# Optimization experiments

Measured on AMD Instinct MI355X. Metric: run time of the kernel, lower is better.

The kernel has to match this reference:

```python
import jax, jax.numpy as jnp
import numpy as np

B = 262144      # Monte Carlo samples (batch)
DH = 128        # d_hidden
DM = 4          # concatenated input feature dim (two one-hot spins)


def _glorot(key, shape):
    fan_in, fan_out = shape[0], shape[1]
    lim = jnp.sqrt(6.0 / (fan_in + fan_out)).astype(jnp.float32)
    return jax.random.uniform(key, shape, jnp.float32, -lim, lim)


def setup_inputs() -> dict:
    key = jax.random.key(0)
    ks = jax.random.split(key, 10)
    inputs = jax.random.normal(ks[0], (B, DM), jnp.float32)
    h1 = jax.random.normal(ks[1], (B, DH), jnp.float32)
    h2 = jax.random.normal(ks[2], (B, DH), jnp.float32)
    U1 = _glorot(ks[3], (DH, DH))
    U2 = _glorot(ks[4], (DH, DH))
    # flax GRUCell params: input kernels (with bias), hidden kernels
    # (r,z: no bias; n: bias). Packed as [ir|iz|in] and [hr|hz].
    Wi = _glorot(ks[5], (DM, 3 * DH))
    bi = jnp.zeros((3 * DH,), jnp.float32)
    Whrz = _glorot(ks[6], (DH, 2 * DH))
    Whn = _glorot(ks[7], (DH, DH))
    bhn = jnp.zeros((DH,), jnp.float32)
    return {"inputs": inputs, "h1": h1, "h2": h2, "U1": U1, "U2": U2,
            "Wi": Wi, "bi": bi, "Whrz": Whrz, "Whn": Whn, "bhn": bhn}


def reference(inputs, h1, h2, U1, U2, Wi, bi, Whrz, Whn, bhn):
    # Fuse the two neighbor hidden states: h = h1 @ U1 + h2 @ U2
    h = h1 @ U1 + h2 @ U2                      # [B, DH]
    # flax GRUCell(carry=h, inputs=x):
    i_proj = inputs @ Wi + bi                  # [B, 3*DH]
    ir, iz, i_n = jnp.split(i_proj, 3, axis=-1)
    hrz = h @ Whrz                             # [B, 2*DH] (no bias in flax)
    hr, hz = jnp.split(hrz, 2, axis=-1)
    r = jax.nn.sigmoid(ir + hr)
    z = jax.nn.sigmoid(iz + hz)
    n = jnp.tanh(i_n + r * (h @ Whn + bhn))
    new_h = (1.0 - z) * n + z * h
    return (new_h, new_h)
```

## Files before the change

### kernel.cpp

```cpp
#include <hip/hip_runtime.h>

using bf8 = __attribute__((ext_vector_type(8))) short;
using bf4 = __attribute__((ext_vector_type(4))) short;
using f4  = __attribute__((ext_vector_type(4))) float;
using u16 = unsigned short;
using u64 = unsigned long long;

#define NROWS 262144

#define FLAG_B   0
#define PU_B     128
#define PV_B     (PU_B + 65536)
#define PWI_B    (PV_B + 196608)
#define BHN_B    (PWI_B + 24576)

#define N_PU   32768
#define N_PV   98304
#define N_PWI  12288
#define PACK_ITEMS (N_PU + N_PV + N_PWI + 128)

static __device__ __forceinline__ float bf2f(u16 u) {
    unsigned v = ((unsigned)u) << 16;
    return __builtin_bit_cast(float, v);
}
static __device__ __forceinline__ u16 f2bf(float f) {
    unsigned x = __builtin_bit_cast(unsigned, f);
    x = x + 0x7fffu + ((x >> 16) & 1u);
    return (u16)(x >> 16);
}

template<bool FP32>
static __device__ __forceinline__ u16 ldw(const void* p, int i) {
    if constexpr (FP32) return f2bf(((const float*)p)[i]);
    else                return ((const u16*)p)[i];
}
template<bool FP32>
static __device__ __forceinline__ float ldf(const void* p, int i) {
    if constexpr (FP32) return ((const float*)p)[i];
    else                return bf2f(((const u16*)p)[i]);
}
template<bool FP32>
static __device__ __forceinline__ bf8 ld8(const void* base, int idx) {
    if constexpr (!FP32) {
        return *(const bf8*)((const u16*)base + idx);
    } else {
        const float* f = (const float*)base + idx;
        f4 u = *(const f4*)f;
        f4 v = *(const f4*)(f + 4);
        bf8 r;
        r[0]=(short)f2bf(u[0]); r[1]=(short)f2bf(u[1]); r[2]=(short)f2bf(u[2]); r[3]=(short)f2bf(u[3]);
        r[4]=(short)f2bf(v[0]); r[5]=(short)f2bf(v[1]); r[6]=(short)f2bf(v[2]); r[7]=(short)f2bf(v[3]);
        return r;
    }
}

__global__ void detect_mode(const u16* __restrict__ h1u, int* __restrict__ flag) {
    if (threadIdx.x == 0 && blockIdx.x == 0) {
        int huge = 0;
#pragma unroll 8
        for (int i = 0; i < 256; ++i) {
            u16 v = h1u[i * 2];
            huge += (((v >> 7) & 0xFF) >= 0xC0);
        }
        *flag = (huge > 0) ? 1 : 0;
    }
}

template<bool FP32>
__global__ void prep_pack(const void* __restrict__ U1, const void* __restrict__ U2,
                          const void* __restrict__ Whrz, const void* __restrict__ Whn,
                          const void* __restrict__ Wi, const void* __restrict__ bi,
                          const void* __restrict__ bhn, char* __restrict__ ws,
                          const int* __restrict__ flag)
{
    if ((*flag != 0) != FP32) return;
    int e = blockIdx.x * 256 + threadIdx.x;
    if (e >= PACK_ITEMS) return;
    u16*   pU   = (u16*)(ws + PU_B);
    u16*   pV   = (u16*)(ws + PV_B);
    u16*   pWi  = (u16*)(ws + PWI_B);
    float* bhnF = (float*)(ws + BHN_B);
    if (e < N_PU) {
        int j = e & 7, lane = (e >> 3) & 63, f = e >> 9;
        int kb = f & 7, nt = f >> 3;
        int k = kb * 32 + (lane >> 4) * 8 + j;
        int n = nt * 16 + (lane & 15);
        pU[e] = (k < 128) ? ldw<FP32>(U1, k * 128 + n) : ldw<FP32>(U2, (k - 128) * 128 + n);
    } else if (e < N_PU + N_PV) {
        int e2 = e - N_PU;
        int j = e2 & 7, lane = (e2 >> 3) & 63, f = e2 >> 9;
        int kb = f & 7, nt = f >> 3;
        int k = kb * 32 + (lane >> 4) * 8 + j;
        int n = nt * 16 + (lane & 15);
        const void* Us = (k < 128) ? U1 : U2;
        int krow = (k < 128) ? k : k - 128;
        float acc = 0.f;
        if (n < 256) {
#pragma unroll 8
            for (int j2 = 0; j2 < 128; ++j2)
                acc = fmaf(ldf<FP32>(Us, krow * 128 + j2), ldf<FP32>(Whrz, j2 * 256 + n), acc);
        } else {
#pragma unroll 8
            for (int j2 = 0; j2 < 128; ++j2)
                acc = fmaf(ldf<FP32>(Us, krow * 128 + j2), ldf<FP32>(Whn, j2 * 128 + (n - 256)), acc);
        }
        pV[e2] = f2bf(acc);
    } else if (e < N_PU + N_PV + N_PWI) {
        int e3 = e - (N_PU + N_PV);
        int j = e3 & 7, lane = (e3 >> 3) & 63, nt = e3 >> 9;
        int k = (lane >> 4) * 8 + j;
        int n = nt * 16 + (lane & 15);
        u16 v = 0;
        if (k < 4)       v = ldw<FP32>(Wi, k * 384 + n);
        else if (k == 4) v = ldw<FP32>(bi, n);
        pWi[e3] = v;
    } else {
        int i = e - (N_PU + N_PV + N_PWI);
        bhnF[i] = ldf<FP32>(bhn, i);
    }
}

template<bool FP32>
__global__ __launch_bounds__(256, 3) void gru_fused(
    const void* __restrict__ xin, const void* __restrict__ h1,
    const void* __restrict__ h2, const char* __restrict__ ws,
    void* __restrict__ out, const int* __restrict__ flag, int write2)
{
    if ((*flag != 0) != FP32) return;
    const int tid = threadIdx.x;
    const int w  = tid >> 6;
    const int l  = tid & 63;
    const int q  = l >> 4;
    const int lr = l & 15;
    const int g0 = blockIdx.x * 128 + w * 32;

    const bf8* __restrict__ pU  = (const bf8*)(ws + PU_B);
    const bf8* __restrict__ pV  = (const bf8*)(ws + PV_B);
    const bf8* __restrict__ pWi = (const bf8*)(ws + PWI_B);
    const float* __restrict__ bhnF = (const float*)(ws + BHN_B);

    bf8 a[2][8];
#pragma unroll
    for (int m = 0; m < 2; ++m) {
        int row = g0 + m * 16 + lr;
        int base = row * 128 + q * 8;
#pragma unroll
        for (int kb = 0; kb < 4; ++kb) {
            a[m][kb]     = ld8<FP32>(h1, base + kb * 32);
            a[m][kb + 4] = ld8<FP32>(h2, base + kb * 32);
        }
    }

    bf8 ax[2];
#pragma unroll
    for (int m = 0; m < 2; ++m) {
        bf8 v = {0,0,0,0,0,0,0,0};
        if (q == 0) {
            int row = g0 + m * 16 + lr;
            if constexpr (FP32) {
                f4 xv = *(const f4*)((const float*)xin + row * 4);
#pragma unroll
                for (int k = 0; k < 4; ++k) v[k] = (short)f2bf(xv[k]);
            } else {
                bf4 xv = *(const bf4*)((const u16*)xin + row * 4);
#pragma unroll
                for (int k = 0; k < 4; ++k) v[k] = xv[k];
            }
            v[4] = (short)0x3F80;
        }
        ax[m] = v;
    }

    float* outF = (float*)out;
    u16*   outB = (u16*)out;

#pragma unroll 1
    for (int nt = 0; nt < 8; ++nt) {
        const f4 z4 = {0.f, 0.f, 0.f, 0.f};
        f4 aH[2], aR[2], aZ[2], aN[2], aI[2];
        bf8 biR = pWi[(nt     ) * 64 + l];
        bf8 biZ = pWi[(nt + 8 ) * 64 + l];
        bf8 biN = pWi[(nt + 16) * 64 + l];
#pragma unroll
        for (int m = 0; m < 2; ++m) {
            aH[m] = z4;
            aN[m] = z4;
            aR[m] = __builtin_amdgcn_mfma_f32_16x16x32_bf16(biR, ax[m], z4, 0, 0, 0);
            aZ[m] = __builtin_amdgcn_mfma_f32_16x16x32_bf16(biZ, ax[m], z4, 0, 0, 0);
            aI[m] = __builtin_amdgcn_mfma_f32_16x16x32_bf16(biN, ax[m], z4, 0, 0, 0);
        }
#pragma unroll
        for (int kb = 0; kb < 8; ++kb) {
            bf8 bH = pU[(nt * 8 + kb) * 64 + l];
            bf8 bR = pV[((nt     ) * 8 + kb) * 64 + l];
            bf8 bZ = pV[((nt + 8 ) * 8 + kb) * 64 + l];
            bf8 bN = pV[((nt + 16) * 8 + kb) * 64 + l];
#pragma unroll
            for (int m = 0; m < 2; ++m) {
                aH[m] = __builtin_amdgcn_mfma_f32_16x16x32_bf16(bH, a[m][kb], aH[m], 0, 0, 0);
                aR[m] = __builtin_amdgcn_mfma_f32_16x16x32_bf16(bR, a[m][kb], aR[m], 0, 0, 0);
                aZ[m] = __builtin_amdgcn_mfma_f32_16x16x32_bf16(bZ, a[m][kb], aZ[m], 0, 0, 0);
                aN[m] = __builtin_amdgcn_mfma_f32_16x16x32_bf16(bN, a[m][kb], aN[m], 0, 0, 0);
            }
        }
        int c0 = nt * 16 + q * 4;
        f4 bh4 = *(const f4*)(bhnF + c0);
#pragma unroll
        for (int m = 0; m < 2; ++m) {
            int row = g0 + m * 16 + lr;
            f4 o;
#pragma unroll
            for (int i = 0; i < 4; ++i) {
                float hv = aH[m][i];
                float sr = fminf(fmaxf(aR[m][i], -30.f), 30.f);
                float r  = __fdividef(1.f, 1.f + __expf(-sr));
                float sz = fminf(fmaxf(aZ[m][i], -30.f), 30.f);
                float z  = __fdividef(1.f, 1.f + __expf(-sz));
                float t  = aI[m][i] + r * (aN[m][i] + bh4[i]);
                t = fminf(fmaxf(t, -15.f), 15.f);
                float e2t = __expf(2.f * t);
                float n = (e2t - 1.f) * __fdividef(1.f, e2t + 1.f);
                o[i] = (1.f - z) * n + z * hv;
            }
            int off = row * 128 + c0;
            if constexpr (FP32) {
                *(f4*)(outF + off) = o;
                if (write2) *(f4*)(outF + NROWS * 128 + off) = o;
            } else {
                unsigned lo = (unsigned)f2bf(o[0]) | ((unsigned)f2bf(o[1]) << 16);
                unsigned hi = (unsigned)f2bf(o[2]) | ((unsigned)f2bf(o[3]) << 16);
                u64 pk = ((u64)hi << 32) | lo;
                *(u64*)(outB + off) = pk;
                if (write2) *(u64*)(outB + NROWS * 128 + off) = pk;
            }
        }
    }
}

extern "C" void kernel_launch(void* const* d_in, const int* in_sizes, int n_in,
                              void* d_out, int out_size, void* d_ws, size_t ws_size,
                              hipStream_t stream) {
    const void* x    = d_in[0];
    const void* h1   = d_in[1];
    const void* h2   = d_in[2];
    const void* U1   = d_in[3];
    const void* U2   = d_in[4];
    const void* Wi   = d_in[5];
    const void* bi   = d_in[6];
    const void* Whrz = d_in[7];
    const void* Whn  = d_in[8];
    const void* bhn  = d_in[9];
    char* ws   = (char*)d_ws;
    int* flag  = (int*)(ws + FLAG_B);
    int write2 = (out_size >= 2 * NROWS * 128) ? 1 : 0;

    detect_mode<<<1, 64, 0, stream>>>((const u16*)h1, flag);
    const int pblk = (PACK_ITEMS + 255) / 256;
    prep_pack<false><<<pblk, 256, 0, stream>>>(U1, U2, Whrz, Whn, Wi, bi, bhn, ws, flag);
    prep_pack<true ><<<pblk, 256, 0, stream>>>(U1, U2, Whrz, Whn, Wi, bi, bhn, ws, flag);
    gru_fused<false><<<NROWS / 128, 256, 0, stream>>>(x, h1, h2, ws, d_out, flag, write2);
    gru_fused<true ><<<NROWS / 128, 256, 0, stream>>>(x, h1, h2, ws, d_out, flag, write2);
}
```

Before: 586.8 us.

## Stage packed weight tiles into LDS with double-buffered async loads

Each block now grows to 512 threads (8 waves) and cooperatively copies the packed U/V weight fragments for the next column tile into a double-buffered shared-memory area using global_load_lds, while the current tile is computed from LDS. This replaces per-wave global/L2 reads of the same weights with one shared copy per block and overlaps the weight fetch with the MFMA work. In exchange it adds a block-wide barrier every tile iteration and uses 64KB of LDS per block, which may limit how many blocks fit on a CU. There is no explicit wait on the async LDS writes before the barrier, so correctness relies on the compiler inserting the counter wait.

```diff
diff --git a/kernel.cpp b/kernel.cpp
--- a/kernel.cpp
+++ b/kernel.cpp
@@ -121,21 +121,21 @@
 }
 
 template<bool FP32>
-__global__ __launch_bounds__(256, 3) void gru_fused(
+__global__ __launch_bounds__(512, 3) void gru_fused(
     const void* __restrict__ xin, const void* __restrict__ h1,
     const void* __restrict__ h2, const char* __restrict__ ws,
     void* __restrict__ out, const int* __restrict__ flag, int write2)
 {
     if ((*flag != 0) != FP32) return;
+    __shared__ __align__(16) u16 smem[2][16384];
     const int tid = threadIdx.x;
     const int w  = tid >> 6;
     const int l  = tid & 63;
     const int q  = l >> 4;
     const int lr = l & 15;
-    const int g0 = blockIdx.x * 128 + w * 32;
-
-    const bf8* __restrict__ pU  = (const bf8*)(ws + PU_B);
-    const bf8* __restrict__ pV  = (const bf8*)(ws + PV_B);
+    const int g0 = blockIdx.x * 256 + w * 32;
+
+    const char* __restrict__ wsc = ws;
     const bf8* __restrict__ pWi = (const bf8*)(ws + PWI_B);
     const float* __restrict__ bhnF = (const float*)(ws + BHN_B);
 
@@ -171,11 +171,35 @@
         ax[m] = v;
     }
 
+    auto stage = [&](int buf, int nt) {
+#pragma unroll
+        for (int r = 0; r < 4; ++r) {
+            int s = w * 4 + r;
+            int gb;
+            if (s < 8) {
+                gb = PU_B + (nt * 8 + s) * 1024;
+            } else {
+                int g = (s - 8) >> 3, kb = (s - 8) & 7;
+                gb = PV_B + ((nt + g * 8) * 8 + kb) * 1024;
+            }
+            __builtin_amdgcn_global_load_lds(
+                (const __attribute__((address_space(1))) unsigned int*)(wsc + gb + l * 16),
+                (__attribute__((address_space(3))) unsigned int*)(&smem[buf][s * 512]),
+                16, 0, 0);
+        }
+    };
+
     float* outF = (float*)out;
     u16*   outB = (u16*)out;
 
+    stage(0, 0);
+    __syncthreads();
+
+    int buf = 0;
 #pragma unroll 1
     for (int nt = 0; nt < 8; ++nt) {
+        if (nt < 7) stage(buf ^ 1, nt + 1);
+
         const f4 z4 = {0.f, 0.f, 0.f, 0.f};
         f4 aH[2], aR[2], aZ[2], aN[2], aI[2];
         bf8 biR = pWi[(nt     ) * 64 + l];
@@ -189,12 +213,13 @@
             aZ[m] = __builtin_amdgcn_mfma_f32_16x16x32_bf16(biZ, ax[m], z4, 0, 0, 0);
             aI[m] = __builtin_amdgcn_mfma_f32_16x16x32_bf16(biN, ax[m], z4, 0, 0, 0);
         }
+        const u16* sb = &smem[buf][0];
 #pragma unroll
         for (int kb = 0; kb < 8; ++kb) {
-            bf8 bH = pU[(nt * 8 + kb) * 64 + l];
-            bf8 bR = pV[((nt     ) * 8 + kb) * 64 + l];
-            bf8 bZ = pV[((nt + 8 ) * 8 + kb) * 64 + l];
-            bf8 bN = pV[((nt + 16) * 8 + kb) * 64 + l];
+            bf8 bH = *(const bf8*)(sb + (kb     ) * 512 + l * 8);
+            bf8 bR = *(const bf8*)(sb + (kb +  8) * 512 + l * 8);
+            bf8 bZ = *(const bf8*)(sb + (kb + 16) * 512 + l * 8);
+            bf8 bN = *(const bf8*)(sb + (kb + 24) * 512 + l * 8);
 #pragma unroll
             for (int m = 0; m < 2; ++m) {
                 aH[m] = __builtin_amdgcn_mfma_f32_16x16x32_bf16(bH, a[m][kb], aH[m], 0, 0, 0);
@@ -234,6 +259,8 @@
                 if (write2) *(u64*)(outB + NROWS * 128 + off) = pk;
             }
         }
+        __syncthreads();
+        buf ^= 1;
     }
 }
 
@@ -258,6 +285,6 @@
     const int pblk = (PACK_ITEMS + 255) / 256;
     prep_pack<false><<<pblk, 256, 0, stream>>>(U1, U2, Whrz, Whn, Wi, bi, bhn, ws, flag);
     prep_pack<true ><<<pblk, 256, 0, stream>>>(U1, U2, Whrz, Whn, Wi, bi, bhn, ws, flag);
-    gru_fused<false><<<NROWS / 128, 256, 0, stream>>>(x, h1, h2, ws, d_out, flag, write2);
-    gru_fused<true ><<<NROWS / 128, 256, 0, stream>>>(x, h1, h2, ws, d_out, flag, write2);
-}
+    gru_fused<false><<<NROWS / 256, 512, 0, stream>>>(x, h1, h2, ws, d_out, flag, write2);
+    gru_fused<true ><<<NROWS / 256, 512, 0, stream>>>(x, h1, h2, ws, d_out, flag, write2);
+}
```

Result: no change. 597.3 us (+1.8%).

## Stage GRU outputs through LDS for coalesced nontemporal stores, loop m outer

Applied to the files above, without the earlier changes.

The loop order changes so each wave processes one 16-row tile at a time across all 8 column tiles. This halves the live accumulators, and launch bounds rise to 4 waves per SIMD. Per-tile results are staged in a padded per-wave LDS buffer and then written out as fully coalesced row-contiguous vectors with nontemporal stores. The aim is to cut scattered partial-row writes and raise occupancy. In exchange the B-fragment weight loads are repeated for each m, and extra LDS traffic is added.

```diff
diff --git a/kernel.cpp b/kernel.cpp
--- a/kernel.cpp
+++ b/kernel.cpp
@@ -121,12 +121,13 @@
 }
 
 template<bool FP32>
-__global__ __launch_bounds__(256, 3) void gru_fused(
+__global__ __launch_bounds__(256, 4) void gru_fused(
     const void* __restrict__ xin, const void* __restrict__ h1,
     const void* __restrict__ h2, const char* __restrict__ ws,
     void* __restrict__ out, const int* __restrict__ flag, int write2)
 {
     if ((*flag != 0) != FP32) return;
+    __shared__ __align__(16) float so[4][16][132];
     const int tid = threadIdx.x;
     const int w  = tid >> 6;
     const int l  = tid & 63;
@@ -175,63 +176,64 @@
     u16*   outB = (u16*)out;
 
 #pragma unroll 1
-    for (int nt = 0; nt < 8; ++nt) {
-        const f4 z4 = {0.f, 0.f, 0.f, 0.f};
-        f4 aH[2], aR[2], aZ[2], aN[2], aI[2];
-        bf8 biR = pWi[(nt     ) * 64 + l];
-        bf8 biZ = pWi[(nt + 8 ) * 64 + l];
-        bf8 biN = pWi[(nt + 16) * 64 + l];
-#pragma unroll
-        for (int m = 0; m < 2; ++m) {
-            aH[m] = z4;
-            aN[m] = z4;
-            aR[m] = __builtin_amdgcn_mfma_f32_16x16x32_bf16(biR, ax[m], z4, 0, 0, 0);
-            aZ[m] = __builtin_amdgcn_mfma_f32_16x16x32_bf16(biZ, ax[m], z4, 0, 0, 0);
-            aI[m] = __builtin_amdgcn_mfma_f32_16x16x32_bf16(biN, ax[m], z4, 0, 0, 0);
-        }
-#pragma unroll
-        for (int kb = 0; kb < 8; ++kb) {
-            bf8 bH = pU[(nt * 8 + kb) * 64 + l];
-            bf8 bR = pV[((nt     ) * 8 + kb) * 64 + l];
-            bf8 bZ = pV[((nt + 8 ) * 8 + kb) * 64 + l];
-            bf8 bN = pV[((nt + 16) * 8 + kb) * 64 + l];
-#pragma unroll
-            for (int m = 0; m < 2; ++m) {
-                aH[m] = __builtin_amdgcn_mfma_f32_16x16x32_bf16(bH, a[m][kb], aH[m], 0, 0, 0);
-                aR[m] = __builtin_amdgcn_mfma_f32_16x16x32_bf16(bR, a[m][kb], aR[m], 0, 0, 0);
-                aZ[m] = __builtin_amdgcn_mfma_f32_16x16x32_bf16(bZ, a[m][kb], aZ[m], 0, 0, 0);
-                aN[m] = __builtin_amdgcn_mfma_f32_16x16x32_bf16(bN, a[m][kb], aN[m], 0, 0, 0);
-            }
-        }
-        int c0 = nt * 16 + q * 4;
-        f4 bh4 = *(const f4*)(bhnF + c0);
-#pragma unroll
-        for (int m = 0; m < 2; ++m) {
-            int row = g0 + m * 16 + lr;
+    for (int m = 0; m < 2; ++m) {
+#pragma unroll 1
+        for (int nt = 0; nt < 8; ++nt) {
+            const f4 z4 = {0.f, 0.f, 0.f, 0.f};
+            f4 aH, aR, aZ, aN, aI;
+            bf8 biR = pWi[(nt     ) * 64 + l];
+            bf8 biZ = pWi[(nt + 8 ) * 64 + l];
+            bf8 biN = pWi[(nt + 16) * 64 + l];
+            aH = z4;
+            aN = z4;
+            aR = __builtin_amdgcn_mfma_f32_16x16x32_bf16(biR, ax[m], z4, 0, 0, 0);
+            aZ = __builtin_amdgcn_mfma_f32_16x16x32_bf16(biZ, ax[m], z4, 0, 0, 0);
+            aI = __builtin_amdgcn_mfma_f32_16x16x32_bf16(biN, ax[m], z4, 0, 0, 0);
+#pragma unroll
+            for (int kb = 0; kb < 8; ++kb) {
+                bf8 bH = pU[(nt * 8 + kb) * 64 + l];
+                bf8 bR = pV[((nt     ) * 8 + kb) * 64 + l];
+                bf8 bZ = pV[((nt + 8 ) * 8 + kb) * 64 + l];
+                bf8 bN = pV[((nt + 16) * 8 + kb) * 64 + l];
+                aH = __builtin_amdgcn_mfma_f32_16x16x32_bf16(bH, a[m][kb], aH, 0, 0, 0);
+                aR = __builtin_amdgcn_mfma_f32_16x16x32_bf16(bR, a[m][kb], aR, 0, 0, 0);
+                aZ = __builtin_amdgcn_mfma_f32_16x16x32_bf16(bZ, a[m][kb], aZ, 0, 0, 0);
+                aN = __builtin_amdgcn_mfma_f32_16x16x32_bf16(bN, a[m][kb], aN, 0, 0, 0);
+            }
+            int c0 = nt * 16 + q * 4;
+            f4 bh4 = *(const f4*)(bhnF + c0);
             f4 o;
 #pragma unroll
             for (int i = 0; i < 4; ++i) {
-                float hv = aH[m][i];
-                float sr = fminf(fmaxf(aR[m][i], -30.f), 30.f);
+                float hv = aH[i];
+                float sr = fminf(fmaxf(aR[i], -30.f), 30.f);
                 float r  = __fdividef(1.f, 1.f + __expf(-sr));
-                float sz = fminf(fmaxf(aZ[m][i], -30.f), 30.f);
+                float sz = fminf(fmaxf(aZ[i], -30.f), 30.f);
                 float z  = __fdividef(1.f, 1.f + __expf(-sz));
-                float t  = aI[m][i] + r * (aN[m][i] + bh4[i]);
+                float t  = aI[i] + r * (aN[i] + bh4[i]);
                 t = fminf(fmaxf(t, -15.f), 15.f);
                 float e2t = __expf(2.f * t);
                 float n = (e2t - 1.f) * __fdividef(1.f, e2t + 1.f);
                 o[i] = (1.f - z) * n + z * hv;
             }
-            int off = row * 128 + c0;
+            *(f4*)&so[w][lr][c0] = o;
+        }
+#pragma unroll
+        for (int p = 0; p < 8; ++p) {
+            int ch  = p * 64 + l;
+            int row = ch >> 5;
+            int c4  = ch & 31;
+            f4 v = *(const f4*)&so[w][row][c4 * 4];
+            int off = (g0 + m * 16 + row) * 128 + c4 * 4;
             if constexpr (FP32) {
-                *(f4*)(outF + off) = o;
-                if (write2) *(f4*)(outF + NROWS * 128 + off) = o;
+                __builtin_nontemporal_store(v, (f4*)(outF + off));
+                if (write2) __builtin_nontemporal_store(v, (f4*)(outF + NROWS * 128 + off));
             } else {
-                unsigned lo = (unsigned)f2bf(o[0]) | ((unsigned)f2bf(o[1]) << 16);
-                unsigned hi = (unsigned)f2bf(o[2]) | ((unsigned)f2bf(o[3]) << 16);
+                unsigned lo = (unsigned)f2bf(v[0]) | ((unsigned)f2bf(v[1]) << 16);
+                unsigned hi = (unsigned)f2bf(v[2]) | ((unsigned)f2bf(v[3]) << 16);
                 u64 pk = ((u64)hi << 32) | lo;
-                *(u64*)(outB + off) = pk;
-                if (write2) *(u64*)(outB + NROWS * 128 + off) = pk;
+                __builtin_nontemporal_store(pk, (u64*)(outB + off));
+                if (write2) __builtin_nontemporal_store(pk, (u64*)(outB + NROWS * 128 + off));
             }
         }
     }
```

Result: slower. 632.2 us (+7.7%).
